# Kernel optimization log

Hardware: AMD Instinct MI355X
Metric: run time of the kernel (lower is better)

The kernel has to match this reference:

```python
import jax, jax.numpy as jnp
import numpy as np
jax.config.update("jax_enable_x64", True)

B, S, E, H, L, FF = 2, 1024, 768, 12, 4, 2048
MAX_THOUGHT_LEN = 3
LN_EPS = 1e-5

def _sinusoidal_pe(max_len, d):
    pos = np.arange(max_len)[:, None]
    div = np.exp(np.arange(0, d, 2) * (-np.log(10000.0) / d))
    pe = np.zeros((max_len, d), np.float32)
    pe[:, 0::2] = np.sin(pos * div)
    pe[:, 1::2] = np.cos(pos * div)
    return jnp.asarray(pe)

def _build_mask(Smax, thoughts_taken, n_tokens):
    # Vectorized equivalent of the torch loop building the block-causal mask.
    bs = thoughts_taken + 1
    i = np.arange(Smax)[:, None]
    j = np.arange(Smax)[None, :]
    same_block = (i // bs == j // bs) & (i // bs < n_tokens) & ((i % bs) >= (j % bs))
    start_vis = ((j % bs) == 0) & (j // bs < n_tokens) & (i > j) & (i < n_tokens * bs)
    allowed = same_block | start_vis
    # TransformerEncoder canonicalizes the bool mask: True (disallowed) -> -inf additive
    return jnp.asarray(np.where(allowed, 0.0, -np.inf).astype(np.float64))

def _layernorm(x, w, b):
    mu = jnp.mean(x, -1, keepdims=True)
    var = jnp.mean((x - mu) ** 2, -1, keepdims=True)
    return (x - mu) / jnp.sqrt(var + LN_EPS) * w + b

def setup_inputs() -> dict:
    key = jax.random.key(0)
    ks = jax.random.split(key, 8)
    f32 = jnp.float32
    return {
        "x": jax.random.normal(ks[0], (B, S, E), f32),
        "padding_mask": jnp.zeros((B, S), bool),
        "thought_pe": jax.random.normal(ks[1], (MAX_THOUGHT_LEN + 1, E), f32),
        "Wqkv": jax.random.normal(ks[2], (L, 3 * E, E), f32) * (E ** -0.5),
        "bqkv": jnp.zeros((L, 3 * E), f32),
        "W1": jax.random.normal(ks[3], (L, FF, E), f32) * (E ** -0.5),
        "b1": jnp.zeros((L, FF), f32),
        "W2": jax.random.normal(ks[4], (L, E, FF), f32) * (FF ** -0.5),
        "b2": jnp.zeros((L, E), f32),
        "ln1_w": jnp.ones((L, E), f32), "ln1_b": jnp.zeros((L, E), f32),
        "ln2_w": jnp.ones((L, E), f32), "ln2_b": jnp.zeros((L, E), f32),
        "lnf_w": jnp.ones((E,), f32), "lnf_b": jnp.zeros((E,), f32),
        "thoughts_taken": 1,
        "real_token_count": 512,
    }

def reference(x, padding_mask, thought_pe, Wqkv, bqkv, W1, b1, W2, b2,
              ln1_w, ln1_b, ln2_w, ln2_b, lnf_w, lnf_b,
              thoughts_taken, real_token_count):
    # NOTE: padding_mask is accepted but unused, matching the custom layer.
    nt = thoughts_taken + 1
    pe = _sinusoidal_pe(S, E)
    # DualPositionalEncoding (eval mode -> dropout is identity)
    h = x[:, : real_token_count * nt].reshape(B, real_token_count, nt, E)
    h = h + pe[:real_token_count][None, :, None, :] + thought_pe[:nt][None, None, :, :]
    h = h.reshape(B, real_token_count * nt, E)
    pad = S - real_token_count * nt
    if pad > 0:
        h = jnp.pad(h, ((0, 0), (0, pad), (0, 0)))
    mask = _build_mask(S, thoughts_taken, real_token_count)
    scale = 1.0 / jnp.sqrt(jnp.float64(E // H))
    for l in range(L):
        # manual fp64 attention, exactly as the torch layer
        s64 = h.astype(jnp.float64)
        qkv = s64 @ Wqkv[l].astype(jnp.float64).T + bqkv[l].astype(jnp.float64)
        q, k, v = jnp.split(qkv, 3, axis=-1)
        rh = lambda t: t.reshape(B, S, H, E // H).transpose(0, 2, 1, 3)
        q, k, v = rh(q), rh(k), rh(v)
        scores = jnp.einsum("bhqd,bhkd->bhqk", q, k) * scale + mask
        attn = jax.nn.softmax(scores, axis=-1)
        ao = jnp.einsum("bhqk,bhkd->bhqd", attn, v).transpose(0, 2, 1, 3).reshape(B, S, E)
        # NOTE: no out_proj -- the custom forward skips self_attn.out_proj
        h = _layernorm(h + ao.astype(h.dtype), ln1_w[l], ln1_b[l])
        ff = jax.nn.gelu(h @ W1[l].T + b1[l], approximate=False) @ W2[l].T + b2[l]
        h = _layernorm(h + ff, ln2_w[l], ln2_b[l])
        h = jnp.nan_to_num(h)
    return _layernorm(h, lnf_w, lnf_b)
```

## Files before the change

kernel.cpp:

```cpp
#include <hip/hip_runtime.h>
#include <math.h>

#define SEQ 1024
#define EMB 768
#define NHEAD 12
#define HDIM 64
#define NLAYER 4
#define FFDIM 2048
#define BATCH 2
#define ROWS (BATCH * SEQ)
#define BH (BATCH * NHEAD)
#define NCHUNK 4

using f16 = _Float16;
using f16x4 = __attribute__((ext_vector_type(4))) _Float16;
using f16x8 = __attribute__((ext_vector_type(8))) _Float16;
using f32x4 = __attribute__((ext_vector_type(4))) float;
using f32x16 = __attribute__((ext_vector_type(16))) float;
typedef unsigned long long u64;

__device__ inline void gload16(const void* g, void* l) {
    __builtin_amdgcn_global_load_lds((const __attribute__((address_space(1))) unsigned*)g,
                                     (__attribute__((address_space(3))) unsigned*)l, 16, 0, 0);
}

__global__ void embed_kernel(const float* __restrict__ x,
                             const float* __restrict__ tpe,
                             float* __restrict__ h32,
                             f16* __restrict__ h16,
                             const int* __restrict__ tt_p,
                             const int* __restrict__ rtc_p) {
    int idx = blockIdx.x * blockDim.x + threadIdx.x;
    if (idx >= BATCH * SEQ * EMB) return;
    int e = idx % EMB;
    int s = (idx / EMB) % SEQ;
    int nt = *tt_p + 1;
    int rtc = *rtc_p;
    float val;
    if (s < rtc * nt) {
        int p = s / nt;
        int t = s % nt;
        int i2 = e & ~1;
        float div = __expf((float)i2 * -0.0119926314f);
        float ang = (float)p * div;
        float pe = (e & 1) ? __cosf(ang) : __sinf(ang);
        val = x[idx] + pe + tpe[t * EMB + e];
    } else {
        val = 0.0f;
    }
    h32[idx] = val;
    h16[idx] = (f16)val;
}

__global__ void build_mask(u64* __restrict__ mtab,
                           const int* __restrict__ tt_p,
                           const int* __restrict__ rtc_p) {
    int idx = blockIdx.x * blockDim.x + threadIdx.x;
    if (idx >= SEQ * 16) return;
    int i = idx >> 4, jt = idx & 15;
    int nt = *tt_p + 1, rtc = *rtc_p;
    int id = i / nt, im = i % nt;
    int iok = (i < rtc * nt);
    u64 m = 0;
    for (int k = 0; k < 64; k++) {
        int j = jt * 64 + k;
        int jd = j / nt, jm = j % nt;
        bool same = (id == jd) && (id < rtc) && (im >= jm);
        bool sv   = (jm == 0) && (jd < rtc) && (i > j) && iok;
        if (same || sv) m |= (1ull << k);
    }
    mtab[idx] = m;
}

__global__ void cast3(const float* __restrict__ a, int na,
                      const float* __restrict__ b, int nb,
                      const float* __restrict__ c, int nc,
                      f16* __restrict__ oa, f16* __restrict__ ob, f16* __restrict__ oc) {
    int total = na + nb + nc;
    for (int i = blockIdx.x * blockDim.x + threadIdx.x; i < total;
         i += gridDim.x * blockDim.x) {
        const float* src;
        f16* dst;
        int off;
        if (i < na)            { src = a; dst = oa; off = i; }
        else if (i < na + nb)  { src = b; dst = ob; off = i - na; }
        else                   { src = c; dst = oc; off = i - na - nb; }
        float4 v = ((const float4*)src)[off];
        f16x4 o;
        o[0] = (f16)v.x; o[1] = (f16)v.y; o[2] = (f16)v.z; o[3] = (f16)v.w;
        ((f16x4*)dst)[off] = o;
    }
}

template<int ACT, int OUT>
__global__ __launch_bounds__(256) void gemm_f16(const f16* __restrict__ A,
                                                const f16* __restrict__ W,
                                                const float* __restrict__ bias,
                                                f16* __restrict__ Ch,
                                                f16* __restrict__ vtg,
                                                int M, int N, int K) {
    __shared__ f16 As[128 * 64];
    __shared__ f16 Ws[128 * 64];
    const int tid = threadIdx.x, lane = tid & 63, wave = tid >> 6;
    const int gx = gridDim.x;
    const int nwg = gx * gridDim.y;
    int orig = blockIdx.y * gx + blockIdx.x;
    int nid = (nwg & 7) ? orig : ((orig & 7) * (nwg >> 3) + (orig >> 3));
    const int bm = (nid / gx) * 128, bn = (nid % gx) * 128;
    const int l31 = lane & 31, l32 = lane >> 5;
    const int wm = (wave >> 1) * 64, wn = (wave & 1) * 64;
    const int srow = lane >> 3, sslot = lane & 7;
    const int klen = K / gridDim.z;
    const int kbeg = blockIdx.z * klen, kend = kbeg + klen;

    f32x16 acc[2][2];
#pragma unroll
    for (int mi = 0; mi < 2; mi++)
#pragma unroll
        for (int ni = 0; ni < 2; ni++)
#pragma unroll
            for (int e = 0; e < 16; e++) acc[mi][ni][e] = 0.f;

    for (int k0 = kbeg; k0 < kend; k0 += 64) {
#pragma unroll
        for (int i = 0; i < 4; i++) {
            int R0 = wave * 32 + i * 8;
            int row = R0 + srow;
            int gs = (sslot ^ (row & 7)) << 3;
            gload16(A + (size_t)(bm + row) * K + k0 + gs, As + R0 * 64);
            gload16(W + (size_t)(bn + row) * K + k0 + gs, Ws + R0 * 64);
        }
        __syncthreads();
#pragma unroll
        for (int ks = 0; ks < 4; ks++) {
            int kslot = ks * 2 + l32;
            f16x8 a[2], b[2];
#pragma unroll
            for (int mi = 0; mi < 2; mi++) {
                int row = wm + mi * 32 + l31;
                a[mi] = *(const f16x8*)(As + row * 64 + ((kslot ^ (row & 7)) << 3));
            }
#pragma unroll
            for (int ni = 0; ni < 2; ni++) {
                int row = wn + ni * 32 + l31;
                b[ni] = *(const f16x8*)(Ws + row * 64 + ((kslot ^ (row & 7)) << 3));
            }
#pragma unroll
            for (int mi = 0; mi < 2; mi++)
#pragma unroll
                for (int ni = 0; ni < 2; ni++)
                    acc[mi][ni] = __builtin_amdgcn_mfma_f32_32x32x16_f16(a[mi], b[ni], acc[mi][ni], 0, 0, 0);
        }
        __syncthreads();
    }

#pragma unroll
    for (int ni = 0; ni < 2; ni++) {
        int nbase = bn + wn + ni * 32;
        int n = nbase + l31;
        if (OUT == 3) {
            f16* dst = Ch + (size_t)blockIdx.z * ROWS * N;
#pragma unroll
            for (int mi = 0; mi < 2; mi++)
#pragma unroll
                for (int reg = 0; reg < 16; reg++) {
                    int m = bm + wm + mi * 32 + (reg & 3) + 8 * (reg >> 2) + 4 * l32;
                    dst[(size_t)m * N + n] = (f16)acc[mi][ni][reg];
                }
        } else {
            float bv = bias[n];
            if (OUT != 2 || nbase < 2 * EMB) {
                int cstride = (OUT == 2) ? 2 * EMB : N;
#pragma unroll
                for (int mi = 0; mi < 2; mi++) {
#pragma unroll
                    for (int reg = 0; reg < 16; reg++) {
                        int m = bm + wm + mi * 32 + (reg & 3) + 8 * (reg >> 2) + 4 * l32;
                        float v = acc[mi][ni][reg] + bv;
                        if (ACT) v = 0.5f * v * (1.0f + erff(v * 0.70710678118654752f));
                        Ch[(size_t)m * cstride + n] = (f16)v;
                    }
                }
            } else {
                int d = n - 2 * EMB;
                int hh = d >> 6, dd = d & 63;
#pragma unroll
                for (int mi = 0; mi < 2; mi++) {
#pragma unroll
                    for (int q = 0; q < 4; q++) {
                        int m0 = bm + wm + mi * 32 + 8 * q + 4 * l32;
                        int bb = m0 >> 10, s0 = m0 & (SEQ - 1);
                        f16x4 pack;
#pragma unroll
                        for (int r = 0; r < 4; r++) pack[r] = (f16)(acc[mi][ni][4 * q + r] + bv);
                        *(f16x4*)(vtg + ((size_t)((bb * NHEAD + hh) * HDIM + dd)) * SEQ + s0) = pack;
                    }
                }
            }
        }
    }
}

__global__ __launch_bounds__(256) void attn_part(const f16* __restrict__ qk,
                                                 const f16* __restrict__ vtg,
                                                 const u64* __restrict__ mtab,
                                                 f16* __restrict__ po,
                                                 float* __restrict__ pm,
                                                 float* __restrict__ pl) {
    const int c = blockIdx.x;
    const int qt = blockIdx.y;
    if (c * 4 > qt) return;
    const int bh = blockIdx.z;
    const int b = bh / NHEAD, hh = bh % NHEAD;
    const int q0 = qt * 64;
    const int jt_beg = c * 4, jt_end = min(qt, c * 4 + 3);

    __shared__ f16 Qs[64 * 64];
    __shared__ f16 Ks[2][64 * 64];
    __shared__ f16 VT[2][64 * 64];
    __shared__ f16 Ps[4 * 16 * 64];

    const int tid = threadIdx.x, lane = tid & 63, wave = tid >> 6;
    const int l15 = lane & 15, l16 = lane >> 4;
    const int RS = 2 * EMB;
    const f16* vth = vtg + (size_t)(b * NHEAD + hh) * HDIM * SEQ;
    const float SCALE2 = 0.125f * 1.44269504088896f;

#pragma unroll
    for (int it = 0; it < 2; it++) {
        int R0 = wave * 16 + it * 8;
        int row = R0 + (lane >> 3), slot = lane & 7;
        int gs = (slot ^ (row & 7)) << 3;
        gload16(qk + (size_t)(b * SEQ + q0 + row) * RS + hh * HDIM + gs, Qs + R0 * 64);
        gload16(qk + (size_t)(b * SEQ + jt_beg * 64 + row) * RS + EMB + hh * HDIM + gs,
                Ks[0] + R0 * 64);
        gload16(vth + (size_t)row * SEQ + jt_beg * 64 + gs, VT[0] + R0 * 64);
    }
    __syncthreads();

    f16x8 qa[2];
#pragma unroll
    for (int ks = 0; ks < 2; ks++) {
        int row = wave * 16 + l15;
        int kslot = l16 + ks * 4;
        qa[ks] = *(const f16x8*)(Qs + row * 64 + ((kslot ^ (row & 7)) << 3));
    }

    float mrow[4], lsum[4];
    f32x4 o[4];
    int iglob[4];
#pragma unroll
    for (int r = 0; r < 4; r++) {
        mrow[r] = -1e30f; lsum[r] = 0.f;
        iglob[r] = q0 + wave * 16 + l16 * 4 + r;
    }
#pragma unroll
    for (int nf = 0; nf < 4; nf++) o[nf] = (f32x4){0.f, 0.f, 0.f, 0.f};

    for (int jt = jt_beg; jt <= jt_end; jt++) {
        const int cur = (jt - jt_beg) & 1;
        if (jt < jt_end) {
            const int nxt = cur ^ 1;
            const int jn0 = (jt + 1) * 64;
#pragma unroll
            for (int it = 0; it < 2; it++) {
                int R0 = wave * 16 + it * 8;
                int row = R0 + (lane >> 3), slot = lane & 7;
                int gs = (slot ^ (row & 7)) << 3;
                gload16(qk + (size_t)(b * SEQ + jn0 + row) * RS + EMB + hh * HDIM + gs,
                        Ks[nxt] + R0 * 64);
                gload16(vth + (size_t)row * SEQ + jn0 + gs, VT[nxt] + R0 * 64);
            }
        }

        unsigned mlo[4], mhi[4];
#pragma unroll
        for (int r = 0; r < 4; r++) {
            u64 mk = mtab[iglob[r] * 16 + jt];
            mlo[r] = (unsigned)mk;
            mhi[r] = (unsigned)(mk >> 32);
        }

        f32x4 s[4];
        __builtin_amdgcn_s_setprio(1);
#pragma unroll
        for (int nf = 0; nf < 4; nf++) {
            s[nf] = (f32x4){0.f, 0.f, 0.f, 0.f};
#pragma unroll
            for (int ks = 0; ks < 2; ks++) {
                int row = nf * 16 + l15;
                int kslot = l16 + ks * 4;
                f16x8 kb = *(const f16x8*)(Ks[cur] + row * 64 + ((kslot ^ (row & 7)) << 3));
                s[nf] = __builtin_amdgcn_mfma_f32_16x16x32_f16(qa[ks], kb, s[nf], 0, 0, 0);
            }
        }
        __builtin_amdgcn_s_setprio(0);

        float p[4][4];
        float tmax[4] = {-1e30f, -1e30f, -1e30f, -1e30f};
#pragma unroll
        for (int nf = 0; nf < 4; nf++) {
            int sh = (nf & 1) * 16 + l15;
#pragma unroll
            for (int r = 0; r < 4; r++) {
                unsigned w = (nf & 2) ? mhi[r] : mlo[r];
                bool allowed = (w >> sh) & 1;
                float val = allowed ? s[nf][r] * SCALE2 : -1e30f;
                p[nf][r] = val;
                tmax[r] = fmaxf(tmax[r], val);
            }
        }
#pragma unroll
        for (int r = 0; r < 4; r++) {
            tmax[r] = fmaxf(tmax[r], __shfl_xor(tmax[r], 1));
            tmax[r] = fmaxf(tmax[r], __shfl_xor(tmax[r], 2));
            tmax[r] = fmaxf(tmax[r], __shfl_xor(tmax[r], 4));
            tmax[r] = fmaxf(tmax[r], __shfl_xor(tmax[r], 8));
        }
        float alpha[4], rsum[4], meff[4];
#pragma unroll
        for (int r = 0; r < 4; r++) {
            float mn = fmaxf(mrow[r], tmax[r]);
            alpha[r] = exp2f(mrow[r] - mn);
            mrow[r] = mn;
            meff[r] = (mn <= -1e29f) ? 0.f : mn;
            rsum[r] = 0.f;
        }
#pragma unroll
        for (int nf = 0; nf < 4; nf++)
#pragma unroll
            for (int r = 0; r < 4; r++) {
                float e = exp2f(p[nf][r] - meff[r]);
                p[nf][r] = e;
                rsum[r] += e;
            }
#pragma unroll
        for (int r = 0; r < 4; r++) {
            rsum[r] += __shfl_xor(rsum[r], 1);
            rsum[r] += __shfl_xor(rsum[r], 2);
            rsum[r] += __shfl_xor(rsum[r], 4);
            rsum[r] += __shfl_xor(rsum[r], 8);
            lsum[r] = lsum[r] * alpha[r] + rsum[r];
        }
#pragma unroll
        for (int nf = 0; nf < 4; nf++)
#pragma unroll
            for (int r = 0; r < 4; r++) o[nf][r] *= alpha[r];

        f16* P = Ps + wave * 16 * 64;
#pragma unroll
        for (int nf = 0; nf < 4; nf++)
#pragma unroll
            for (int r = 0; r < 4; r++) {
                int prow = l16 * 4 + r;
                int pcol = nf * 16 + l15;
                P[prow * 64 + (((pcol >> 3) ^ (prow & 7)) << 3) + (pcol & 7)] = (f16)p[nf][r];
            }

        __builtin_amdgcn_s_setprio(1);
#pragma unroll
        for (int ks = 0; ks < 2; ks++) {
            int kslot = l16 + ks * 4;
            int prow = l15;
            f16x8 pa = *(const f16x8*)(P + prow * 64 + ((kslot ^ (prow & 7)) << 3));
#pragma unroll
            for (int nf = 0; nf < 4; nf++) {
                int vrow = nf * 16 + l15;
                f16x8 vb = *(const f16x8*)(VT[cur] + vrow * 64 + ((kslot ^ (vrow & 7)) << 3));
                o[nf] = __builtin_amdgcn_mfma_f32_16x16x32_f16(pa, vb, o[nf], 0, 0, 0);
            }
        }
        __builtin_amdgcn_s_setprio(0);
        __syncthreads();
    }

    const size_t base = (size_t)(c * BH + bh) * SEQ;
#pragma unroll
    for (int r = 0; r < 4; r++) {
        int i = q0 + wave * 16 + l16 * 4 + r;
#pragma unroll
        for (int nf = 0; nf < 4; nf++)
            po[(base + i) * 64 + nf * 16 + l15] = (f16)o[nf][r];
        if (l15 == 0) {
            pm[base + i] = mrow[r];
            pl[base + i] = lsum[r];
        }
    }
}

__global__ __launch_bounds__(256) void add_ln_attn(const float* __restrict__ X,
                                                   const f16* __restrict__ po,
                                                   const float* __restrict__ pm,
                                                   const float* __restrict__ pl,
                                                   const float* __restrict__ w,
                                                   const float* __restrict__ bsh,
                                                   float* __restrict__ out32,
                                                   f16* __restrict__ out16) {
    const int row = blockIdx.x * 4 + (threadIdx.x >> 6);
    const int lane = threadIdx.x & 63;
    const int b = row >> 10, i = row & (SEQ - 1);
    const int nch = (i >> 6) / 4 + 1;
    const float* xr = X + (size_t)row * EMB;
    float4 v[3];
    float s = 0.f;
#pragma unroll
    for (int t = 0; t < 3; t++) {
        int e = t * 256 + lane * 4;
        int hh = e >> 6, d = e & 63;
        size_t hbase = (size_t)(b * NHEAD + hh) * SEQ + i;
        float m = -1e30f;
        for (int c = 0; c < nch; c++) m = fmaxf(m, pm[hbase + (size_t)c * BH * SEQ]);
        float meff = (m <= -1e29f) ? 0.f : m;
        float lt = 0.f;
        float4 ov = {0.f, 0.f, 0.f, 0.f};
        for (int c = 0; c < nch; c++) {
            size_t idx = hbase + (size_t)c * BH * SEQ;
            float wgt = exp2f(pm[idx] - meff);
            lt += pl[idx] * wgt;
            f16x4 pv = *(const f16x4*)(po + idx * 64 + d);
            ov.x += (float)pv[0] * wgt; ov.y += (float)pv[1] * wgt;
            ov.z += (float)pv[2] * wgt; ov.w += (float)pv[3] * wgt;
        }
        float inv = (lt > 0.f) ? 1.0f / lt : 0.0f;
        float4 a = *(const float4*)(xr + e);
        a.x += ov.x * inv; a.y += ov.y * inv; a.z += ov.z * inv; a.w += ov.w * inv;
        v[t] = a;
        s += a.x + a.y + a.z + a.w;
    }
#pragma unroll
    for (int k = 1; k < 64; k <<= 1) s += __shfl_xor(s, k);
    float mu = s * (1.0f / EMB);
    float s2 = 0.f;
#pragma unroll
    for (int t = 0; t < 3; t++) {
        float dx = v[t].x - mu, dy = v[t].y - mu, dz = v[t].z - mu, dw = v[t].w - mu;
        s2 += dx * dx + dy * dy + dz * dz + dw * dw;
    }
#pragma unroll
    for (int k = 1; k < 64; k <<= 1) s2 += __shfl_xor(s2, k);
    float inv = rsqrtf(s2 * (1.0f / EMB) + 1e-5f);
#pragma unroll
    for (int t = 0; t < 3; t++) {
        int e = t * 256 + lane * 4;
        float4 wv = *(const float4*)(w + e);
        float4 bv = *(const float4*)(bsh + e);
        float4 o;
        o.x = (v[t].x - mu) * inv * wv.x + bv.x;
        o.y = (v[t].y - mu) * inv * wv.y + bv.y;
        o.z = (v[t].z - mu) * inv * wv.z + bv.z;
        o.w = (v[t].w - mu) * inv * wv.w + bv.w;
        *(float4*)(out32 + (size_t)row * EMB + e) = o;
        f16x4 hh;
        hh[0] = (f16)o.x; hh[1] = (f16)o.y; hh[2] = (f16)o.z; hh[3] = (f16)o.w;
        *(f16x4*)(out16 + (size_t)row * EMB + e) = hh;
    }
}

__global__ __launch_bounds__(256) void add_ln_split4(const float* __restrict__ X,
                                                     const f16* __restrict__ part,
                                                     const float* __restrict__ bias,
                                                     const float* __restrict__ w,
                                                     const float* __restrict__ bsh,
                                                     float* __restrict__ out32,
                                                     f16* __restrict__ out16) {
    const int row = blockIdx.x * 4 + (threadIdx.x >> 6);
    const int lane = threadIdx.x & 63;
    const float* xr = X + (size_t)row * EMB;
    float4 v[3];
    float s = 0.f;
#pragma unroll
    for (int t = 0; t < 3; t++) {
        int e = t * 256 + lane * 4;
        float4 a = *(const float4*)(xr + e);
        float4 bb = *(const float4*)(bias + e);
        a.x += bb.x; a.y += bb.y; a.z += bb.z; a.w += bb.w;
#pragma unroll
        for (int z = 0; z < 4; z++) {
            f16x4 pz = *(const f16x4*)(part + (size_t)z * ROWS * EMB + (size_t)row * EMB + e);
            a.x += (float)pz[0]; a.y += (float)pz[1];
            a.z += (float)pz[2]; a.w += (float)pz[3];
        }
        v[t] = a;
        s += a.x + a.y + a.z + a.w;
    }
#pragma unroll
    for (int k = 1; k < 64; k <<= 1) s += __shfl_xor(s, k);
    float mu = s * (1.0f / EMB);
    float s2 = 0.f;
#pragma unroll
    for (int t = 0; t < 3; t++) {
        float dx = v[t].x - mu, dy = v[t].y - mu, dz = v[t].z - mu, dw = v[t].w - mu;
        s2 += dx * dx + dy * dy + dz * dz + dw * dw;
    }
#pragma unroll
    for (int k = 1; k < 64; k <<= 1) s2 += __shfl_xor(s2, k);
    float inv = rsqrtf(s2 * (1.0f / EMB) + 1e-5f);
#pragma unroll
    for (int t = 0; t < 3; t++) {
        int e = t * 256 + lane * 4;
        float4 wv = *(const float4*)(w + e);
        float4 bv = *(const float4*)(bsh + e);
        float4 o;
        o.x = (v[t].x - mu) * inv * wv.x + bv.x;
        o.y = (v[t].y - mu) * inv * wv.y + bv.y;
        o.z = (v[t].z - mu) * inv * wv.z + bv.z;
        o.w = (v[t].w - mu) * inv * wv.w + bv.w;
        *(float4*)(out32 + (size_t)row * EMB + e) = o;
        f16x4 hh;
        hh[0] = (f16)o.x; hh[1] = (f16)o.y; hh[2] = (f16)o.z; hh[3] = (f16)o.w;
        *(f16x4*)(out16 + (size_t)row * EMB + e) = hh;
    }
}

__global__ __launch_bounds__(256) void ln_final(const float* __restrict__ X,
                                                const float* __restrict__ w,
                                                const float* __restrict__ bsh,
                                                float* __restrict__ out32) {
    const int row = blockIdx.x * 4 + (threadIdx.x >> 6);
    const int lane = threadIdx.x & 63;
    const float* xr = X + (size_t)row * EMB;
    float4 v[3];
    float s = 0.f;
#pragma unroll
    for (int t = 0; t < 3; t++) {
        int e = t * 256 + lane * 4;
        v[t] = *(const float4*)(xr + e);
        s += v[t].x + v[t].y + v[t].z + v[t].w;
    }
#pragma unroll
    for (int k = 1; k < 64; k <<= 1) s += __shfl_xor(s, k);
    float mu = s * (1.0f / EMB);
    float s2 = 0.f;
#pragma unroll
    for (int t = 0; t < 3; t++) {
        float dx = v[t].x - mu, dy = v[t].y - mu, dz = v[t].z - mu, dw = v[t].w - mu;
        s2 += dx * dx + dy * dy + dz * dz + dw * dw;
    }
#pragma unroll
    for (int k = 1; k < 64; k <<= 1) s2 += __shfl_xor(s2, k);
    float inv = rsqrtf(s2 * (1.0f / EMB) + 1e-5f);
#pragma unroll
    for (int t = 0; t < 3; t++) {
        int e = t * 256 + lane * 4;
        float4 wv = *(const float4*)(w + e);
        float4 bv = *(const float4*)(bsh + e);
        float4 o;
        o.x = (v[t].x - mu) * inv * wv.x + bv.x;
        o.y = (v[t].y - mu) * inv * wv.y + bv.y;
        o.z = (v[t].z - mu) * inv * wv.z + bv.z;
        o.w = (v[t].w - mu) * inv * wv.w + bv.w;
        *(float4*)(out32 + (size_t)row * EMB + e) = o;
    }
}

extern "C" void kernel_launch(void* const* d_in, const int* in_sizes, int n_in,
                              void* d_out, int out_size, void* d_ws, size_t ws_size,
                              hipStream_t stream) {
    const float* x      = (const float*)d_in[0];
    const float* tpe    = (const float*)d_in[2];
    const float* Wqkv   = (const float*)d_in[3];
    const float* bqkv   = (const float*)d_in[4];
    const float* W1     = (const float*)d_in[5];
    const float* b1     = (const float*)d_in[6];
    const float* W2     = (const float*)d_in[7];
    const float* b2     = (const float*)d_in[8];
    const float* ln1_w  = (const float*)d_in[9];
    const float* ln1_b  = (const float*)d_in[10];
    const float* ln2_w  = (const float*)d_in[11];
    const float* ln2_b  = (const float*)d_in[12];
    const float* lnf_w  = (const float*)d_in[13];
    const float* lnf_b  = (const float*)d_in[14];
    const int*   tt     = (const int*)d_in[15];
    const int*   rtc    = (const int*)d_in[16];
    float* out = (float*)d_out;

    char* wsp = (char*)d_ws;
    float* h32  = (float*)wsp;
    f16*   h16  = (f16*)(wsp + 6291456);
    f16*   act  = (f16*)(wsp + 9437184);
    f16*   vtg  = (f16*)(wsp + 17825792);
    f16*   part = (f16*)(wsp + 20971520);
    f16*   wbuf = (f16*)(wsp + 33554432);
    f16*   po   = (f16*)(wsp + 72876032);
    float* pm   = (float*)(wsp + 85458944);
    float* pl   = (float*)(wsp + 85852160);
    u64*   mtab = (u64*)(wsp + 86245376);

    const int EQ = 3 * EMB * EMB;
    const int E1 = FFDIM * EMB;
    const int E2 = EMB * FFDIM;
    f16* wqAll = wbuf;
    f16* w1All = wbuf + (size_t)NLAYER * EQ;
    f16* w2All = w1All + (size_t)NLAYER * E1;

    cast3<<<4096, 256, 0, stream>>>(Wqkv, NLAYER * EQ / 4, W1, NLAYER * E1 / 4,
                                    W2, NLAYER * E2 / 4, wqAll, w1All, w2All);
    embed_kernel<<<(BATCH * SEQ * EMB + 255) / 256, 256, 0, stream>>>(x, tpe, h32, h16, tt, rtc);
    build_mask<<<SEQ * 16 / 256, 256, 0, stream>>>(mtab, tt, rtc);

    for (int l = 0; l < NLAYER; l++) {
        const f16* wq16 = wqAll + (size_t)l * EQ;
        const f16* w116 = w1All + (size_t)l * E1;
        const f16* w216 = w2All + (size_t)l * E2;
        const float* bq  = bqkv + (size_t)l * 3 * EMB;
        const float* bb1 = b1 + (size_t)l * FFDIM;
        const float* bb2 = b2 + (size_t)l * EMB;

        gemm_f16<0, 2><<<dim3(3 * EMB / 128, ROWS / 128), 256, 0, stream>>>(
            h16, wq16, bq, act, vtg, ROWS, 3 * EMB, EMB);

        attn_part<<<dim3(NCHUNK, SEQ / 64, BH), 256, 0, stream>>>(act, vtg, mtab, po, pm, pl);

        add_ln_attn<<<ROWS / 4, 256, 0, stream>>>(h32, po, pm, pl,
                                                  ln1_w + l * EMB, ln1_b + l * EMB, h32, h16);

        gemm_f16<1, 1><<<dim3(FFDIM / 128, ROWS / 128), 256, 0, stream>>>(
            h16, w116, bb1, act, nullptr, ROWS, FFDIM, EMB);

        gemm_f16<0, 3><<<dim3(EMB / 128, ROWS / 128, 4), 256, 0, stream>>>(
            act, w216, nullptr, part, nullptr, ROWS, EMB, FFDIM);

        add_ln_split4<<<ROWS / 4, 256, 0, stream>>>(h32, part, bb2,
                                                    ln2_w + l * EMB, ln2_b + l * EMB, h32, h16);
    }

    ln_final<<<ROWS / 4, 256, 0, stream>>>(h32, lnf_w, lnf_b, out);
}
```

Baseline: 450.7 us.

## Split K across two wave groups in QKV and FFN1 GEMMs

Adds a WSPLIT template mode in which a 512-thread block runs two 4-wave groups, each covering half of the K range with its own LDS tiles. The second group writes its accumulators to shared memory and the first group adds them before the epilogue. The goal is more waves per output tile, for better latency hiding, on the QKV and FFN1 GEMMs, whose grids are small relative to the CU count. The cost is double LDS use per block (64KB, which lowers blocks per CU), an extra reduction pass through LDS, and a shorter K loop per group.

```diff
diff --git a/kernel.cpp b/kernel.cpp
--- a/kernel.cpp
+++ b/kernel.cpp
@@ -92,16 +92,20 @@
     }
 }
 
-template<int ACT, int OUT>
-__global__ __launch_bounds__(256) void gemm_f16(const f16* __restrict__ A,
-                                                const f16* __restrict__ W,
-                                                const float* __restrict__ bias,
-                                                f16* __restrict__ Ch,
-                                                f16* __restrict__ vtg,
-                                                int M, int N, int K) {
-    __shared__ f16 As[128 * 64];
-    __shared__ f16 Ws[128 * 64];
-    const int tid = threadIdx.x, lane = tid & 63, wave = tid >> 6;
+template<int ACT, int OUT, int WSPLIT>
+__global__ __launch_bounds__(WSPLIT ? 512 : 256) void gemm_f16(
+        const f16* __restrict__ A,
+        const f16* __restrict__ W,
+        const float* __restrict__ bias,
+        f16* __restrict__ Ch,
+        f16* __restrict__ vtg,
+        int M, int N, int K) {
+    __shared__ f16 smem[(WSPLIT ? 2 : 1) * 2 * 128 * 64];
+    const int tid = threadIdx.x, lane = tid & 63;
+    const int wave = (tid >> 6) & 3;
+    const int group = WSPLIT ? (tid >> 8) : 0;
+    f16* Asg = smem + group * (2 * 128 * 64);
+    f16* Wsg = Asg + 128 * 64;
     const int gx = gridDim.x;
     const int nwg = gx * gridDim.y;
     int orig = blockIdx.y * gx + blockIdx.x;
@@ -111,7 +115,9 @@
     const int wm = (wave >> 1) * 64, wn = (wave & 1) * 64;
     const int srow = lane >> 3, sslot = lane & 7;
     const int klen = K / gridDim.z;
-    const int kbeg = blockIdx.z * klen, kend = kbeg + klen;
+    const int half = WSPLIT ? (klen >> 1) : klen;
+    const int kbeg = blockIdx.z * klen + group * half;
+    const int kend = kbeg + half;
 
     f32x16 acc[2][2];
 #pragma unroll
@@ -127,8 +133,8 @@
             int R0 = wave * 32 + i * 8;
             int row = R0 + srow;
             int gs = (sslot ^ (row & 7)) << 3;
-            gload16(A + (size_t)(bm + row) * K + k0 + gs, As + R0 * 64);
-            gload16(W + (size_t)(bn + row) * K + k0 + gs, Ws + R0 * 64);
+            gload16(A + (size_t)(bm + row) * K + k0 + gs, Asg + R0 * 64);
+            gload16(W + (size_t)(bn + row) * K + k0 + gs, Wsg + R0 * 64);
         }
         __syncthreads();
 #pragma unroll
@@ -138,12 +144,12 @@
 #pragma unroll
             for (int mi = 0; mi < 2; mi++) {
                 int row = wm + mi * 32 + l31;
-                a[mi] = *(const f16x8*)(As + row * 64 + ((kslot ^ (row & 7)) << 3));
+                a[mi] = *(const f16x8*)(Asg + row * 64 + ((kslot ^ (row & 7)) << 3));
             }
 #pragma unroll
             for (int ni = 0; ni < 2; ni++) {
                 int row = wn + ni * 32 + l31;
-                b[ni] = *(const f16x8*)(Ws + row * 64 + ((kslot ^ (row & 7)) << 3));
+                b[ni] = *(const f16x8*)(Wsg + row * 64 + ((kslot ^ (row & 7)) << 3));
             }
 #pragma unroll
             for (int mi = 0; mi < 2; mi++)
@@ -152,6 +158,34 @@
                     acc[mi][ni] = __builtin_amdgcn_mfma_f32_32x32x16_f16(a[mi], b[ni], acc[mi][ni], 0, 0, 0);
         }
         __syncthreads();
+    }
+
+    if (WSPLIT) {
+        float* accs = (float*)smem;
+        if (group == 1) {
+#pragma unroll
+            for (int mi = 0; mi < 2; mi++)
+#pragma unroll
+                for (int ni = 0; ni < 2; ni++)
+#pragma unroll
+                    for (int reg = 0; reg < 16; reg++) {
+                        int ml = wm + mi * 32 + (reg & 3) + 8 * (reg >> 2) + 4 * l32;
+                        int nl = wn + ni * 32 + l31;
+                        accs[ml * 128 + nl] = acc[mi][ni][reg];
+                    }
+        }
+        __syncthreads();
+        if (group == 1) return;
+#pragma unroll
+        for (int mi = 0; mi < 2; mi++)
+#pragma unroll
+            for (int ni = 0; ni < 2; ni++)
+#pragma unroll
+                for (int reg = 0; reg < 16; reg++) {
+                    int ml = wm + mi * 32 + (reg & 3) + 8 * (reg >> 2) + 4 * l32;
+                    int nl = wn + ni * 32 + l31;
+                    acc[mi][ni][reg] += accs[ml * 128 + nl];
+                }
     }
 
 #pragma unroll
@@ -606,7 +640,7 @@
         const float* bb1 = b1 + (size_t)l * FFDIM;
         const float* bb2 = b2 + (size_t)l * EMB;
 
-        gemm_f16<0, 2><<<dim3(3 * EMB / 128, ROWS / 128), 256, 0, stream>>>(
+        gemm_f16<0, 2, 1><<<dim3(3 * EMB / 128, ROWS / 128), 512, 0, stream>>>(
             h16, wq16, bq, act, vtg, ROWS, 3 * EMB, EMB);
 
         attn_part<<<dim3(NCHUNK, SEQ / 64, BH), 256, 0, stream>>>(act, vtg, mtab, po, pm, pl);
@@ -614,10 +648,10 @@
         add_ln_attn<<<ROWS / 4, 256, 0, stream>>>(h32, po, pm, pl,
                                                   ln1_w + l * EMB, ln1_b + l * EMB, h32, h16);
 
-        gemm_f16<1, 1><<<dim3(FFDIM / 128, ROWS / 128), 256, 0, stream>>>(
+        gemm_f16<1, 1, 1><<<dim3(FFDIM / 128, ROWS / 128), 512, 0, stream>>>(
             h16, w116, bb1, act, nullptr, ROWS, FFDIM, EMB);
 
-        gemm_f16<0, 3><<<dim3(EMB / 128, ROWS / 128, 4), 256, 0, stream>>>(
+        gemm_f16<0, 3, 0><<<dim3(EMB / 128, ROWS / 128, 4), 256, 0, stream>>>(
             act, w216, nullptr, part, nullptr, ROWS, EMB, FFDIM);
 
         add_ln_split4<<<ROWS / 4, 256, 0, stream>>>(h32, part, bb2,
```

After: 474.0 us. 1.05x slower.
